# Kernel optimization log

Measured on AMD Instinct MI355X. Metric: run time of the kernel, lower is better.

The kernel has to match this reference:

```python
import jax, jax.numpy as jnp
import numpy as np

EPS = 1e-5

def _ln(x, g, b):
    # layer norm over last dim
    m = jnp.mean(x, axis=-1, keepdims=True)
    v = jnp.mean((x - m) ** 2, axis=-1, keepdims=True)
    return (x - m) * jax.lax.rsqrt(v + EPS) * g + b

def setup_inputs() -> dict:
    key = jax.random.key(0)
    ks = jax.random.split(key, 12)
    B, T, E, H, OUT = 128, 256, 64, 128, 1
    GENOME = 1_000_000
    D = 2 * E  # input_size_lstm
    inp = {}
    inp["indices"] = jax.random.randint(ks[0], (B, T, 2), 0, GENOME, dtype=jnp.int64)
    inp["h0"] = jax.random.normal(ks[1], (B, H), dtype=jnp.float32)
    inp["c0"] = jax.random.normal(ks[2], (B, H), dtype=jnp.float32)
    inp["embed_table"] = jax.random.normal(ks[3], (GENOME, E), dtype=jnp.float32)
    s_ih = 1.0 / np.sqrt(D)
    s_hh = 1.0 / np.sqrt(H)
    inp["W_ih"] = jax.random.uniform(ks[4], (4 * H, D), minval=-s_ih, maxval=s_ih, dtype=jnp.float32)
    inp["W_hh"] = jax.random.uniform(ks[5], (4 * H, H), minval=-s_hh, maxval=s_hh, dtype=jnp.float32)
    inp["g_ih"] = jnp.ones((4 * H,), jnp.float32)
    inp["b_ih"] = jnp.zeros((4 * H,), jnp.float32)
    inp["g_hh"] = jnp.ones((4 * H,), jnp.float32)
    inp["b_hh"] = jnp.zeros((4 * H,), jnp.float32)
    inp["g_c"] = jnp.ones((H,), jnp.float32)
    inp["b_c"] = jnp.zeros((H,), jnp.float32)
    s_o = 1.0 / np.sqrt(H * T)
    inp["W_out"] = jax.random.uniform(ks[6], (OUT * T, H * T), minval=-s_o, maxval=s_o, dtype=jnp.float32)
    inp["b_out"] = jax.random.uniform(ks[7], (OUT * T,), minval=-s_o, maxval=s_o, dtype=jnp.float32)
    return inp

def _forward(indices, embed_table, W_ih, W_hh, g_ih, b_ih, g_hh, b_hh, g_c, b_c, W_out, b_out, h0, c0):
    B, T = indices.shape[0], indices.shape[1]
    H = h0.shape[-1]
    # embedding gather: (B,T,2,E) -> (B,T,2E)
    emb = embed_table[indices].reshape(B, T, -1)
    # precompute input-to-hidden gates for all timesteps: (B,T,4H)
    x_gates = jnp.einsum("btd,gd->btg", emb, W_ih)

    def step(carry, xg):
        h, c = carry
        gates = _ln(xg, g_ih, b_ih) + _ln(h @ W_hh.T, g_hh, b_hh)
        i, f, g, o = jnp.split(gates, 4, axis=-1)
        c_new = jax.nn.sigmoid(f) * c + jax.nn.sigmoid(i) * jnp.tanh(g)
        h_new = jax.nn.sigmoid(o) * jnp.tanh(_ln(c_new, g_c, b_c))
        return (h_new, c_new), h_new

    (_, _), hs = jax.lax.scan(step, (h0, c0), jnp.swapaxes(x_gates, 0, 1))
    # hs: (T,B,H) -> (B,T*H)
    seq_out = jnp.swapaxes(hs, 0, 1).reshape(B, T * H)
    out = jax.nn.sigmoid(seq_out @ W_out.T + b_out)
    return out, emb

def reference(indices, h0, c0, embed_table, W_ih, W_hh, g_ih, b_ih, g_hh, b_hh, g_c, b_c, W_out, b_out):
    return _forward(indices, embed_table, W_ih, W_hh, g_ih, b_ih, g_hh, b_hh, g_c, b_c, W_out, b_out, h0, c0)
```

## Files before the change

kernel.cpp:

```cpp
#include <hip/hip_runtime.h>
#include <cstddef>


typedef __attribute__((ext_vector_type(8))) _Float16 f16x8;
typedef __attribute__((ext_vector_type(4))) float f32x4;

__device__ __forceinline__ float frcp(float x) { return __builtin_amdgcn_rcpf(x); }
__device__ __forceinline__ float sigm(float x) { return frcp(1.0f + __expf(-x)); }
__device__ __forceinline__ float ftanh(float x) {
  float e = __expf(2.0f * x);
  return (e - 1.0f) * frcp(e + 1.0f);
}
__device__ __forceinline__ void split2(float x, unsigned short& hi, unsigned short& lo) {
  _Float16 h = (_Float16)x;
  _Float16 l = (_Float16)((x - (float)h) * 2048.0f);
  hi = *(unsigned short*)&h;
  lo = *(unsigned short*)&l;
}
__device__ __forceinline__ void barrier_lds() {
  asm volatile("s_waitcnt lgkmcnt(0)\n\ts_barrier" ::: "memory");
}

#define SEL4(v, jj) ((jj) == 0 ? (v)[0] : (jj) == 1 ? (v)[1] : (jj) == 2 ? (v)[2] : (v)[3])

__global__ void k_embed(const int* __restrict__ idx, const float4* __restrict__ table4,
                        float4* __restrict__ emb4) {
  int i = blockIdx.x * blockDim.x + threadIdx.x;
  int p = i >> 4, j = i & 15;
  int id = idx[p];
  emb4[(size_t)p * 16 + j] = table4[(size_t)id * 16 + j];
}

__global__ __launch_bounds__(256) void k_gemm_tn(
    const float* __restrict__ A, const float* __restrict__ Bm, float* __restrict__ C,
    int K, int kchunks, int N, size_t partstride)
{
  __shared__ float As[64][65];
  __shared__ float Bs[64][68];
  const int tid = threadIdx.x;
  const int tx = tid & 15, ty = tid >> 4;
  const int m0 = blockIdx.x * 64, n0 = blockIdx.y * 64;
  float acc[4][4] = {};
  size_t kbase = (size_t)blockIdx.z * kchunks * 64;
  for (int kc = 0; kc < kchunks; ++kc) {
    size_t k0 = kbase + (size_t)kc * 64;
    #pragma unroll
    for (int it = 0; it < 4; ++it) {
      int fi = it * 256 + tid;
      int row = fi >> 4, col4 = fi & 15;
      float4 va = *(const float4*)(A + (size_t)(m0 + row) * K + k0 + col4 * 4);
      As[row][col4*4+0] = va.x; As[row][col4*4+1] = va.y;
      As[row][col4*4+2] = va.z; As[row][col4*4+3] = va.w;
      float4 vb = *(const float4*)(Bm + (size_t)(n0 + row) * K + k0 + col4 * 4);
      Bs[col4*4+0][row] = vb.x; Bs[col4*4+1][row] = vb.y;
      Bs[col4*4+2][row] = vb.z; Bs[col4*4+3][row] = vb.w;
    }
    __syncthreads();
    #pragma unroll 8
    for (int k = 0; k < 64; ++k) {
      float a0 = As[ty*4+0][k], a1 = As[ty*4+1][k], a2 = As[ty*4+2][k], a3 = As[ty*4+3][k];
      float b0 = Bs[k][tx*4+0], b1 = Bs[k][tx*4+1], b2 = Bs[k][tx*4+2], b3 = Bs[k][tx*4+3];
      acc[0][0] += a0*b0; acc[0][1] += a0*b1; acc[0][2] += a0*b2; acc[0][3] += a0*b3;
      acc[1][0] += a1*b0; acc[1][1] += a1*b1; acc[1][2] += a1*b2; acc[1][3] += a1*b3;
      acc[2][0] += a2*b0; acc[2][1] += a2*b1; acc[2][2] += a2*b2; acc[2][3] += a2*b3;
      acc[3][0] += a3*b0; acc[3][1] += a3*b1; acc[3][2] += a3*b2; acc[3][3] += a3*b3;
    }
    __syncthreads();
  }
  float* Cp = C + (size_t)blockIdx.z * partstride;
  #pragma unroll
  for (int i = 0; i < 4; ++i) {
    float4 v = make_float4(acc[i][0], acc[i][1], acc[i][2], acc[i][3]);
    *(float4*)(Cp + (size_t)(m0 + ty*4 + i) * N + n0 + tx*4) = v;
  }
}

__global__ __launch_bounds__(256) void k_xln(float4* __restrict__ xg4,
                                             const float4* __restrict__ g4,
                                             const float4* __restrict__ bi4,
                                             const float4* __restrict__ bh4) {
  int row = blockIdx.x * 4 + (threadIdx.x >> 6);
  int lane = threadIdx.x & 63;
  float4* r = xg4 + (size_t)row * 128;
  float4 a = r[lane], b = r[lane + 64];
  float s = a.x + a.y + a.z + a.w + b.x + b.y + b.z + b.w;
  float q = a.x*a.x + a.y*a.y + a.z*a.z + a.w*a.w + b.x*b.x + b.y*b.y + b.z*b.z + b.w*b.w;
  #pragma unroll
  for (int off = 32; off; off >>= 1) { s += __shfl_xor(s, off); q += __shfl_xor(q, off); }
  float m = s * (1.0f / 512.0f);
  float rs = rsqrtf(q * (1.0f / 512.0f) - m * m + 1e-5f);
  float4 ga = g4[lane], gb = g4[64 + lane];
  float4 ia = bi4[lane], ib = bi4[64 + lane];
  float4 ha = bh4[lane], hb = bh4[64 + lane];
  a.x = (a.x - m) * rs * ga.x + ia.x + ha.x; a.y = (a.y - m) * rs * ga.y + ia.y + ha.y;
  a.z = (a.z - m) * rs * ga.z + ia.z + ha.z; a.w = (a.w - m) * rs * ga.w + ia.w + ha.w;
  b.x = (b.x - m) * rs * gb.x + ib.x + hb.x; b.y = (b.y - m) * rs * gb.y + ib.y + hb.y;
  b.z = (b.z - m) * rs * gb.z + ib.z + hb.z; b.w = (b.w - m) * rs * gb.w + ib.w + hb.w;
  r[lane] = a; r[lane + 64] = b;
}

__global__ void k_wprep(const float* __restrict__ Whh, uint4* __restrict__ wfh,
                        uint4* __restrict__ wfl) {
  int i = blockIdx.x * 256 + threadIdx.x;
  int l = i & 63, kc = (i >> 6) & 3, mt = i >> 8;
  int row = mt * 16 + (l & 15);
  int kb = kc * 32 + 8 * (l >> 4);
  float4 a = *(const float4*)(Whh + row * 128 + kb);
  float4 c = *(const float4*)(Whh + row * 128 + kb + 4);
  unsigned short h0,h1,h2,h3,h4,h5,h6,h7, l0,l1,l2,l3,l4,l5,l6,l7;
  split2(a.x,h0,l0); split2(a.y,h1,l1); split2(a.z,h2,l2); split2(a.w,h3,l3);
  split2(c.x,h4,l4); split2(c.y,h5,l5); split2(c.z,h6,l6); split2(c.w,h7,l7);
  uint4 oh, ol;
  oh.x = h0 | ((unsigned)h1 << 16); oh.y = h2 | ((unsigned)h3 << 16);
  oh.z = h4 | ((unsigned)h5 << 16); oh.w = h6 | ((unsigned)h7 << 16);
  ol.x = l0 | ((unsigned)l1 << 16); ol.y = l2 | ((unsigned)l3 << 16);
  ol.z = l4 | ((unsigned)l5 << 16); ol.w = l6 | ((unsigned)l7 << 16);
  wfh[i] = oh; wfl[i] = ol;
}

__global__ __launch_bounds__(512, 2) void k_scan(
    const float* __restrict__ xln,
    const uint4* __restrict__ wfh,
    const uint4* __restrict__ wfl,
    const float* __restrict__ h0, const float* __restrict__ c0,
    const float* __restrict__ g_hh,
    const float* __restrict__ g_c,  const float* __restrict__ b_c,
    float* __restrict__ hs)
{
  const int b = blockIdx.x;
  const int tid = threadIdx.x;
  const int w = tid >> 6, l = tid & 63;
  const int lg = l >> 4;
  const int jj = (l & 15) >> 2;
  const bool wr = (l & 3) == 0;
  const int u = w * 16 + lg * 4 + jj;
  const float inv2048 = 1.0f / 2048.0f;

  __shared__ alignas(16) unsigned short hbh[128];
  __shared__ alignas(16) unsigned short hbl[128];
  __shared__ float2 hred[8];
  __shared__ float2 cred[8];

  uint4 afh0[4], afh1[4], afh2[4], afh3[4];
  uint4 afl0[4], afl1[4], afl2[4], afl3[4];
  #pragma unroll
  for (int kc = 0; kc < 4; ++kc) {
    afh0[kc] = wfh[((w     ) * 4 + kc) * 64 + l];
    afh1[kc] = wfh[((w +  8) * 4 + kc) * 64 + l];
    afh2[kc] = wfh[((w + 16) * 4 + kc) * 64 + l];
    afh3[kc] = wfh[((w + 24) * 4 + kc) * 64 + l];
    afl0[kc] = wfl[((w     ) * 4 + kc) * 64 + l];
    afl1[kc] = wfl[((w +  8) * 4 + kc) * 64 + l];
    afl2[kc] = wfl[((w + 16) * 4 + kc) * 64 + l];
    afl3[kc] = wfl[((w + 24) * 4 + kc) * 64 + l];
  }
  #pragma unroll
  for (int kc = 0; kc < 4; ++kc) {
    asm volatile("" : "+v"(afh0[kc].x), "+v"(afh0[kc].y), "+v"(afh0[kc].z), "+v"(afh0[kc].w));
    asm volatile("" : "+v"(afh1[kc].x), "+v"(afh1[kc].y), "+v"(afh1[kc].z), "+v"(afh1[kc].w));
    asm volatile("" : "+v"(afh2[kc].x), "+v"(afh2[kc].y), "+v"(afh2[kc].z), "+v"(afh2[kc].w));
    asm volatile("" : "+v"(afh3[kc].x), "+v"(afh3[kc].y), "+v"(afh3[kc].z), "+v"(afh3[kc].w));
    asm volatile("" : "+v"(afl0[kc].x), "+v"(afl0[kc].y), "+v"(afl0[kc].z), "+v"(afl0[kc].w));
    asm volatile("" : "+v"(afl1[kc].x), "+v"(afl1[kc].y), "+v"(afl1[kc].z), "+v"(afl1[kc].w));
    asm volatile("" : "+v"(afl2[kc].x), "+v"(afl2[kc].y), "+v"(afl2[kc].z), "+v"(afl2[kc].w));
    asm volatile("" : "+v"(afl3[kc].x), "+v"(afl3[kc].y), "+v"(afl3[kc].z), "+v"(afl3[kc].w));
  }

  const float ghI = g_hh[u], ghF = g_hh[128 + u], ghG = g_hh[256 + u], ghO = g_hh[384 + u];
  const float gcv = g_c[u], bcv = b_c[u];
  float cv = c0[b * 128 + u];
  if (wr) {
    unsigned short hi, lo;
    split2(h0[b * 128 + u], hi, lo);
    hbh[u] = hi; hbl[u] = lo;
  }
  __syncthreads();

  const float* xgb = xln + (size_t)b * 256 * 512;
  float* hsb = hs + (size_t)b * 256 * 128;

  float xI = xgb[u], xF = xgb[128 + u], xG = xgb[256 + u], xO = xgb[384 + u];

  for (int t = 0; t < 256; ++t) {
    const float* xn = xgb + (((t + 1) & 255) << 9);
    float nI = xn[u], nF = xn[128 + u], nG = xn[256 + u], nO = xn[384 + u];

    f32x4 acc0 = {0,0,0,0}, acc1 = {0,0,0,0}, acc2 = {0,0,0,0}, acc3 = {0,0,0,0};
    f32x4 e0 = {0,0,0,0}, e1 = {0,0,0,0}, e2 = {0,0,0,0}, e3 = {0,0,0,0};
    #pragma unroll
    for (int kc = 0; kc < 4; ++kc) {
      uint4 buh = *(const uint4*)((const char*)hbh + kc * 64 + 16 * lg);
      uint4 bul = *(const uint4*)((const char*)hbl + kc * 64 + 16 * lg);
      f16x8 bh = *(f16x8*)&buh;
      f16x8 bl = *(f16x8*)&bul;
      acc0 = __builtin_amdgcn_mfma_f32_16x16x32_f16(*(f16x8*)&afh0[kc], bh, acc0, 0, 0, 0);
      acc1 = __builtin_amdgcn_mfma_f32_16x16x32_f16(*(f16x8*)&afh1[kc], bh, acc1, 0, 0, 0);
      acc2 = __builtin_amdgcn_mfma_f32_16x16x32_f16(*(f16x8*)&afh2[kc], bh, acc2, 0, 0, 0);
      acc3 = __builtin_amdgcn_mfma_f32_16x16x32_f16(*(f16x8*)&afh3[kc], bh, acc3, 0, 0, 0);
      e0 = __builtin_amdgcn_mfma_f32_16x16x32_f16(*(f16x8*)&afh0[kc], bl, e0, 0, 0, 0);
      e1 = __builtin_amdgcn_mfma_f32_16x16x32_f16(*(f16x8*)&afh1[kc], bl, e1, 0, 0, 0);
      e2 = __builtin_amdgcn_mfma_f32_16x16x32_f16(*(f16x8*)&afh2[kc], bl, e2, 0, 0, 0);
      e3 = __builtin_amdgcn_mfma_f32_16x16x32_f16(*(f16x8*)&afh3[kc], bl, e3, 0, 0, 0);
      e0 = __builtin_amdgcn_mfma_f32_16x16x32_f16(*(f16x8*)&afl0[kc], bh, e0, 0, 0, 0);
      e1 = __builtin_amdgcn_mfma_f32_16x16x32_f16(*(f16x8*)&afl1[kc], bh, e1, 0, 0, 0);
      e2 = __builtin_amdgcn_mfma_f32_16x16x32_f16(*(f16x8*)&afl2[kc], bh, e2, 0, 0, 0);
      e3 = __builtin_amdgcn_mfma_f32_16x16x32_f16(*(f16x8*)&afl3[kc], bh, e3, 0, 0, 0);
    }
    f32x4 a0, a1, a2, a3;
    #pragma unroll
    for (int j = 0; j < 4; ++j) {
      a0[j] = acc0[j] + e0[j] * inv2048;
      a1[j] = acc1[j] + e1[j] * inv2048;
      a2[j] = acc2[j] + e2[j] * inv2048;
      a3[j] = acc3[j] + e3[j] * inv2048;
    }

    float s = 0.f, q = 0.f;
    #pragma unroll
    for (int j = 0; j < 4; ++j) {
      s += a0[j] + a1[j] + a2[j] + a3[j];
      q += a0[j]*a0[j] + a1[j]*a1[j] + a2[j]*a2[j] + a3[j]*a3[j];
    }
    s += __shfl_xor(s, 16); s += __shfl_xor(s, 32);
    q += __shfl_xor(q, 16); q += __shfl_xor(q, 32);
    if (l == 0) hred[w] = make_float2(s, q);

    barrier_lds();

    float rsx = 0.f, rsq = 0.f;
    #pragma unroll
    for (int i = 0; i < 8; ++i) { float2 v = hred[i]; rsx += v.x; rsq += v.y; }
    float mh = rsx * (1.0f / 512.0f);
    float rh = rsqrtf(rsq * (1.0f / 512.0f) - mh * mh + 1e-5f);

    float aI = SEL4(a0, jj), aF = SEL4(a1, jj), aG = SEL4(a2, jj), aO = SEL4(a3, jj);
    float gI = xI + (aI - mh) * rh * ghI;
    float gF = xF + (aF - mh) * rh * ghF;
    float gG = xG + (aG - mh) * rh * ghG;
    float gO = xO + (aO - mh) * rh * ghO;

    float cn = sigm(gF) * cv + sigm(gI) * ftanh(gG);
    cv = cn;

    float cs = cn, cq = cn * cn;
    #pragma unroll
    for (int off = 32; off; off >>= 1) { cs += __shfl_xor(cs, off); cq += __shfl_xor(cq, off); }
    if (l == 0) cred[w] = make_float2(cs, cq);

    barrier_lds();

    float tcs = 0.f, tcq = 0.f;
    #pragma unroll
    for (int i = 0; i < 8; ++i) { float2 v = cred[i]; tcs += v.x; tcq += v.y; }
    float mc = tcs * (1.0f / 512.0f);
    float rc = rsqrtf(tcq * (1.0f / 512.0f) - mc * mc + 1e-5f);

    float lnc = (cn - mc) * rc * gcv + bcv;
    float hn = sigm(gO) * ftanh(lnc);

    if (wr) {
      unsigned short hi, lo;
      split2(hn, hi, lo);
      hbh[u] = hi; hbl[u] = lo;
      hsb[(size_t)t * 128 + u] = hn;
    }
    xI = nI; xF = nF; xG = nG; xO = nO;

    barrier_lds();
  }
}

__global__ void k_reduce(const float* __restrict__ part, const float* __restrict__ b_out,
                         float* __restrict__ out) {
  int i = blockIdx.x * 256 + threadIdx.x;
  float s = b_out[i & 255];
  #pragma unroll
  for (int z = 0; z < 32; ++z) s += part[(size_t)z * 32768 + i];
  out[i] = sigm(s);
}

extern "C" void kernel_launch(void* const* d_in, const int* in_sizes, int n_in,
                              void* d_out, int out_size, void* d_ws, size_t ws_size,
                              hipStream_t stream) {
  const int*   idx   = (const int*)  d_in[0];
  const float* h0    = (const float*)d_in[1];
  const float* c0    = (const float*)d_in[2];
  const float* table = (const float*)d_in[3];
  const float* W_ih  = (const float*)d_in[4];
  const float* W_hh  = (const float*)d_in[5];
  const float* g_ih  = (const float*)d_in[6];
  const float* b_ih  = (const float*)d_in[7];
  const float* g_hh  = (const float*)d_in[8];
  const float* b_hh  = (const float*)d_in[9];
  const float* g_c   = (const float*)d_in[10];
  const float* b_c   = (const float*)d_in[11];
  const float* W_out = (const float*)d_in[12];
  const float* b_out = (const float*)d_in[13];

  float* out  = (float*)d_out;
  float* emb  = out + 32768;
  float* ws   = (float*)d_ws;
  float* xg   = ws;
  float* hsb  = ws + 16777216;
  uint4* wfh  = (uint4*)(ws + 20971520);
  uint4* wfl  = (uint4*)(ws + 21004288);
  float* part = ws + 21037056;

  k_embed<<<4096, 256, 0, stream>>>(idx, (const float4*)table, (float4*)emb);
  k_gemm_tn<<<dim3(512, 8, 1), 256, 0, stream>>>(emb, W_ih, xg, 128, 2, 512, 0);
  k_xln<<<8192, 256, 0, stream>>>((float4*)xg, (const float4*)g_ih,
                                  (const float4*)b_ih, (const float4*)b_hh);
  k_wprep<<<32, 256, 0, stream>>>(W_hh, wfh, wfl);
  k_scan<<<128, 512, 0, stream>>>(xg, wfh, wfl, h0, c0, g_hh, g_c, b_c, hsb);
  k_gemm_tn<<<dim3(2, 4, 32), 256, 0, stream>>>(hsb, W_out, part, 32768, 16, 256, 32768);
  k_reduce<<<128, 256, 0, stream>>>(part, b_out, out);
}
```

Measured before the change: 649.4 us.

## Batch four sequences per scan block using spare MFMA columns

The recurrent scan kernel now handles four batch rows per workgroup instead of one. The h-state B operand is laid out so that four of the sixteen MFMA N columns carry distinct batch rows, where before all columns held the same vector. Each lane now processes four hidden units with vectorised loads and stores, and the launch drops from 128 to 32 blocks. The recurrent weight fragments are also pinned to accumulator registers. This cuts redundant matrix and memory work per sequence, at the cost of more elementwise work per lane on the serial per-step critical path and fewer active CUs.

```diff
diff --git a/kernel.cpp b/kernel.cpp
--- a/kernel.cpp
+++ b/kernel.cpp
@@ -20,8 +20,6 @@
 __device__ __forceinline__ void barrier_lds() {
   asm volatile("s_waitcnt lgkmcnt(0)\n\ts_barrier" ::: "memory");
 }
-
-#define SEL4(v, jj) ((jj) == 0 ? (v)[0] : (jj) == 1 ? (v)[1] : (jj) == 2 ? (v)[2] : (v)[3])
 
 __global__ void k_embed(const int* __restrict__ idx, const float4* __restrict__ table4,
                         float4* __restrict__ emb4) {
@@ -127,84 +125,97 @@
     const float* __restrict__ g_c,  const float* __restrict__ b_c,
     float* __restrict__ hs)
 {
-  const int b = blockIdx.x;
+  const int bid = blockIdx.x;
   const int tid = threadIdx.x;
   const int w = tid >> 6, l = tid & 63;
   const int lg = l >> 4;
-  const int jj = (l & 15) >> 2;
-  const bool wr = (l & 3) == 0;
-  const int u = w * 16 + lg * 4 + jj;
+  const int col = l & 15;
+  const bool act = col < 4;
+  const int rclamp = act ? col : 0;
+  const int row = bid * 4 + rclamp;
+  const int u0 = 16 * w + 4 * lg;
   const float inv2048 = 1.0f / 2048.0f;
 
-  __shared__ alignas(16) unsigned short hbh[128];
-  __shared__ alignas(16) unsigned short hbl[128];
-  __shared__ float2 hred[8];
-  __shared__ float2 cred[8];
-
-  uint4 afh0[4], afh1[4], afh2[4], afh3[4];
-  uint4 afl0[4], afl1[4], afl2[4], afl3[4];
+  __shared__ alignas(16) unsigned short hsth[2048];
+  __shared__ alignas(16) unsigned short hstl[2048];
+  __shared__ float2 hred[8][16];
+  __shared__ float2 cred[8][16];
+
+  const f16x8* wh8 = (const f16x8*)wfh;
+  const f16x8* wl8 = (const f16x8*)wfl;
+  f16x8 AH0[4], AH1[4], AH2[4], AH3[4], AL0[4], AL1[4], AL2[4], AL3[4];
   #pragma unroll
   for (int kc = 0; kc < 4; ++kc) {
-    afh0[kc] = wfh[((w     ) * 4 + kc) * 64 + l];
-    afh1[kc] = wfh[((w +  8) * 4 + kc) * 64 + l];
-    afh2[kc] = wfh[((w + 16) * 4 + kc) * 64 + l];
-    afh3[kc] = wfh[((w + 24) * 4 + kc) * 64 + l];
-    afl0[kc] = wfl[((w     ) * 4 + kc) * 64 + l];
-    afl1[kc] = wfl[((w +  8) * 4 + kc) * 64 + l];
-    afl2[kc] = wfl[((w + 16) * 4 + kc) * 64 + l];
-    afl3[kc] = wfl[((w + 24) * 4 + kc) * 64 + l];
+    AH0[kc] = wh8[((w     ) * 4 + kc) * 64 + l];
+    AH1[kc] = wh8[((w +  8) * 4 + kc) * 64 + l];
+    AH2[kc] = wh8[((w + 16) * 4 + kc) * 64 + l];
+    AH3[kc] = wh8[((w + 24) * 4 + kc) * 64 + l];
+    AL0[kc] = wl8[((w     ) * 4 + kc) * 64 + l];
+    AL1[kc] = wl8[((w +  8) * 4 + kc) * 64 + l];
+    AL2[kc] = wl8[((w + 16) * 4 + kc) * 64 + l];
+    AL3[kc] = wl8[((w + 24) * 4 + kc) * 64 + l];
   }
   #pragma unroll
   for (int kc = 0; kc < 4; ++kc) {
-    asm volatile("" : "+v"(afh0[kc].x), "+v"(afh0[kc].y), "+v"(afh0[kc].z), "+v"(afh0[kc].w));
-    asm volatile("" : "+v"(afh1[kc].x), "+v"(afh1[kc].y), "+v"(afh1[kc].z), "+v"(afh1[kc].w));
-    asm volatile("" : "+v"(afh2[kc].x), "+v"(afh2[kc].y), "+v"(afh2[kc].z), "+v"(afh2[kc].w));
-    asm volatile("" : "+v"(afh3[kc].x), "+v"(afh3[kc].y), "+v"(afh3[kc].z), "+v"(afh3[kc].w));
-    asm volatile("" : "+v"(afl0[kc].x), "+v"(afl0[kc].y), "+v"(afl0[kc].z), "+v"(afl0[kc].w));
-    asm volatile("" : "+v"(afl1[kc].x), "+v"(afl1[kc].y), "+v"(afl1[kc].z), "+v"(afl1[kc].w));
-    asm volatile("" : "+v"(afl2[kc].x), "+v"(afl2[kc].y), "+v"(afl2[kc].z), "+v"(afl2[kc].w));
-    asm volatile("" : "+v"(afl3[kc].x), "+v"(afl3[kc].y), "+v"(afl3[kc].z), "+v"(afl3[kc].w));
-  }
-
-  const float ghI = g_hh[u], ghF = g_hh[128 + u], ghG = g_hh[256 + u], ghO = g_hh[384 + u];
-  const float gcv = g_c[u], bcv = b_c[u];
-  float cv = c0[b * 128 + u];
-  if (wr) {
-    unsigned short hi, lo;
-    split2(h0[b * 128 + u], hi, lo);
-    hbh[u] = hi; hbl[u] = lo;
-  }
+    asm volatile("" : "+a"(AH0[kc]), "+a"(AH1[kc]), "+a"(AH2[kc]), "+a"(AH3[kc]));
+    asm volatile("" : "+a"(AL0[kc]), "+a"(AL1[kc]), "+a"(AL2[kc]), "+a"(AL3[kc]));
+  }
+
+  const f32x4 ghI = *(const f32x4*)(g_hh + u0);
+  const f32x4 ghF = *(const f32x4*)(g_hh + 128 + u0);
+  const f32x4 ghG = *(const f32x4*)(g_hh + 256 + u0);
+  const f32x4 ghO = *(const f32x4*)(g_hh + 384 + u0);
+  const f32x4 gc4 = *(const f32x4*)(g_c + u0);
+  const f32x4 bc4 = *(const f32x4*)(b_c + u0);
+  f32x4 cv = *(const f32x4*)(c0 + (size_t)row * 128 + u0);
+
+  #pragma unroll
+  for (int i = tid; i < 1024; i += 512) {
+    ((unsigned int*)hsth)[i] = 0u;
+    ((unsigned int*)hstl)[i] = 0u;
+  }
+  const int kcb = u0 >> 5, lg2 = (u0 >> 3) & 3, i0 = u0 & 7;
+  const int wroff = kcb * 1024 + (lg2 * 16 + col) * 16 + i0 * 2;
   __syncthreads();
-
-  const float* xgb = xln + (size_t)b * 256 * 512;
-  float* hsb = hs + (size_t)b * 256 * 128;
-
-  float xI = xgb[u], xF = xgb[128 + u], xG = xgb[256 + u], xO = xgb[384 + u];
+  if (act) {
+    f32x4 h04 = *(const f32x4*)(h0 + (size_t)row * 128 + u0);
+    unsigned short a_, b_, c_, d_, e_, f_, g_, i_;
+    split2(h04[0], a_, b_); split2(h04[1], c_, d_);
+    split2(h04[2], e_, f_); split2(h04[3], g_, i_);
+    uint2 hv; hv.x = (unsigned)a_ | ((unsigned)c_ << 16); hv.y = (unsigned)e_ | ((unsigned)g_ << 16);
+    uint2 lv; lv.x = (unsigned)b_ | ((unsigned)d_ << 16); lv.y = (unsigned)f_ | ((unsigned)i_ << 16);
+    *(uint2*)((char*)hsth + wroff) = hv;
+    *(uint2*)((char*)hstl + wroff) = lv;
+  }
+  __syncthreads();
+
+  const float* xgb = xln + (size_t)row * 131072;
+  float* hsb = hs + (size_t)row * 32768;
+
+  f32x4 xI = *(const f32x4*)(xgb + u0);
+  f32x4 xF = *(const f32x4*)(xgb + 128 + u0);
+  f32x4 xG = *(const f32x4*)(xgb + 256 + u0);
+  f32x4 xO = *(const f32x4*)(xgb + 384 + u0);
 
   for (int t = 0; t < 256; ++t) {
-    const float* xn = xgb + (((t + 1) & 255) << 9);
-    float nI = xn[u], nF = xn[128 + u], nG = xn[256 + u], nO = xn[384 + u];
-
     f32x4 acc0 = {0,0,0,0}, acc1 = {0,0,0,0}, acc2 = {0,0,0,0}, acc3 = {0,0,0,0};
     f32x4 e0 = {0,0,0,0}, e1 = {0,0,0,0}, e2 = {0,0,0,0}, e3 = {0,0,0,0};
     #pragma unroll
     for (int kc = 0; kc < 4; ++kc) {
-      uint4 buh = *(const uint4*)((const char*)hbh + kc * 64 + 16 * lg);
-      uint4 bul = *(const uint4*)((const char*)hbl + kc * 64 + 16 * lg);
-      f16x8 bh = *(f16x8*)&buh;
-      f16x8 bl = *(f16x8*)&bul;
-      acc0 = __builtin_amdgcn_mfma_f32_16x16x32_f16(*(f16x8*)&afh0[kc], bh, acc0, 0, 0, 0);
-      acc1 = __builtin_amdgcn_mfma_f32_16x16x32_f16(*(f16x8*)&afh1[kc], bh, acc1, 0, 0, 0);
-      acc2 = __builtin_amdgcn_mfma_f32_16x16x32_f16(*(f16x8*)&afh2[kc], bh, acc2, 0, 0, 0);
-      acc3 = __builtin_amdgcn_mfma_f32_16x16x32_f16(*(f16x8*)&afh3[kc], bh, acc3, 0, 0, 0);
-      e0 = __builtin_amdgcn_mfma_f32_16x16x32_f16(*(f16x8*)&afh0[kc], bl, e0, 0, 0, 0);
-      e1 = __builtin_amdgcn_mfma_f32_16x16x32_f16(*(f16x8*)&afh1[kc], bl, e1, 0, 0, 0);
-      e2 = __builtin_amdgcn_mfma_f32_16x16x32_f16(*(f16x8*)&afh2[kc], bl, e2, 0, 0, 0);
-      e3 = __builtin_amdgcn_mfma_f32_16x16x32_f16(*(f16x8*)&afh3[kc], bl, e3, 0, 0, 0);
-      e0 = __builtin_amdgcn_mfma_f32_16x16x32_f16(*(f16x8*)&afl0[kc], bh, e0, 0, 0, 0);
-      e1 = __builtin_amdgcn_mfma_f32_16x16x32_f16(*(f16x8*)&afl1[kc], bh, e1, 0, 0, 0);
-      e2 = __builtin_amdgcn_mfma_f32_16x16x32_f16(*(f16x8*)&afl2[kc], bh, e2, 0, 0, 0);
-      e3 = __builtin_amdgcn_mfma_f32_16x16x32_f16(*(f16x8*)&afl3[kc], bh, e3, 0, 0, 0);
+      f16x8 bh = *(const f16x8*)((const char*)hsth + kc * 1024 + l * 16);
+      f16x8 bl = *(const f16x8*)((const char*)hstl + kc * 1024 + l * 16);
+      acc0 = __builtin_amdgcn_mfma_f32_16x16x32_f16(AH0[kc], bh, acc0, 0, 0, 0);
+      acc1 = __builtin_amdgcn_mfma_f32_16x16x32_f16(AH1[kc], bh, acc1, 0, 0, 0);
+      acc2 = __builtin_amdgcn_mfma_f32_16x16x32_f16(AH2[kc], bh, acc2, 0, 0, 0);
+      acc3 = __builtin_amdgcn_mfma_f32_16x16x32_f16(AH3[kc], bh, acc3, 0, 0, 0);
+      e0 = __builtin_amdgcn_mfma_f32_16x16x32_f16(AH0[kc], bl, e0, 0, 0, 0);
+      e1 = __builtin_amdgcn_mfma_f32_16x16x32_f16(AH1[kc], bl, e1, 0, 0, 0);
+      e2 = __builtin_amdgcn_mfma_f32_16x16x32_f16(AH2[kc], bl, e2, 0, 0, 0);
+      e3 = __builtin_amdgcn_mfma_f32_16x16x32_f16(AH3[kc], bl, e3, 0, 0, 0);
+      e0 = __builtin_amdgcn_mfma_f32_16x16x32_f16(AL0[kc], bh, e0, 0, 0, 0);
+      e1 = __builtin_amdgcn_mfma_f32_16x16x32_f16(AL1[kc], bh, e1, 0, 0, 0);
+      e2 = __builtin_amdgcn_mfma_f32_16x16x32_f16(AL2[kc], bh, e2, 0, 0, 0);
+      e3 = __builtin_amdgcn_mfma_f32_16x16x32_f16(AL3[kc], bh, e3, 0, 0, 0);
     }
     f32x4 a0, a1, a2, a3;
     #pragma unroll
@@ -223,48 +234,61 @@
     }
     s += __shfl_xor(s, 16); s += __shfl_xor(s, 32);
     q += __shfl_xor(q, 16); q += __shfl_xor(q, 32);
-    if (l == 0) hred[w] = make_float2(s, q);
+    if (l < 4) hred[w][l] = make_float2(s, q);
 
     barrier_lds();
 
     float rsx = 0.f, rsq = 0.f;
     #pragma unroll
-    for (int i = 0; i < 8; ++i) { float2 v = hred[i]; rsx += v.x; rsq += v.y; }
+    for (int w2 = 0; w2 < 8; ++w2) { float2 v = hred[w2][col]; rsx += v.x; rsq += v.y; }
     float mh = rsx * (1.0f / 512.0f);
     float rh = rsqrtf(rsq * (1.0f / 512.0f) - mh * mh + 1e-5f);
 
-    float aI = SEL4(a0, jj), aF = SEL4(a1, jj), aG = SEL4(a2, jj), aO = SEL4(a3, jj);
-    float gI = xI + (aI - mh) * rh * ghI;
-    float gF = xF + (aF - mh) * rh * ghF;
-    float gG = xG + (aG - mh) * rh * ghG;
-    float gO = xO + (aO - mh) * rh * ghO;
-
-    float cn = sigm(gF) * cv + sigm(gI) * ftanh(gG);
-    cv = cn;
-
-    float cs = cn, cq = cn * cn;
-    #pragma unroll
-    for (int off = 32; off; off >>= 1) { cs += __shfl_xor(cs, off); cq += __shfl_xor(cq, off); }
-    if (l == 0) cred[w] = make_float2(cs, cq);
+    f32x4 cn;
+    float cs = 0.f, cq = 0.f;
+    #pragma unroll
+    for (int j = 0; j < 4; ++j) {
+      float gI = xI[j] + (a0[j] - mh) * rh * ghI[j];
+      float gF = xF[j] + (a1[j] - mh) * rh * ghF[j];
+      float gG = xG[j] + (a2[j] - mh) * rh * ghG[j];
+      float gO = xO[j] + (a3[j] - mh) * rh * ghO[j];
+      float c_ = sigm(gF) * cv[j] + sigm(gI) * ftanh(gG);
+      cn[j] = c_; cv[j] = c_;
+      xO[j] = gO;
+      cs += c_; cq += c_ * c_;
+    }
+    cs += __shfl_xor(cs, 16); cs += __shfl_xor(cs, 32);
+    cq += __shfl_xor(cq, 16); cq += __shfl_xor(cq, 32);
+    if (l < 4) cred[w][l] = make_float2(cs, cq);
 
     barrier_lds();
 
     float tcs = 0.f, tcq = 0.f;
     #pragma unroll
-    for (int i = 0; i < 8; ++i) { float2 v = cred[i]; tcs += v.x; tcq += v.y; }
-    float mc = tcs * (1.0f / 512.0f);
-    float rc = rsqrtf(tcq * (1.0f / 512.0f) - mc * mc + 1e-5f);
-
-    float lnc = (cn - mc) * rc * gcv + bcv;
-    float hn = sigm(gO) * ftanh(lnc);
-
-    if (wr) {
-      unsigned short hi, lo;
-      split2(hn, hi, lo);
-      hbh[u] = hi; hbl[u] = lo;
-      hsb[(size_t)t * 128 + u] = hn;
-    }
-    xI = nI; xF = nF; xG = nG; xO = nO;
+    for (int w2 = 0; w2 < 8; ++w2) { float2 v = cred[w2][col]; tcs += v.x; tcq += v.y; }
+    float mc = tcs * (1.0f / 128.0f);
+    float rc = rsqrtf(tcq * (1.0f / 128.0f) - mc * mc + 1e-5f);
+
+    f32x4 hn;
+    #pragma unroll
+    for (int j = 0; j < 4; ++j)
+      hn[j] = sigm(xO[j]) * ftanh((cn[j] - mc) * rc * gc4[j] + bc4[j]);
+
+    if (act) {
+      unsigned short a_, b_, c_, d_, e_, f_, g_, i_;
+      split2(hn[0], a_, b_); split2(hn[1], c_, d_);
+      split2(hn[2], e_, f_); split2(hn[3], g_, i_);
+      uint2 hv; hv.x = (unsigned)a_ | ((unsigned)c_ << 16); hv.y = (unsigned)e_ | ((unsigned)g_ << 16);
+      uint2 lv; lv.x = (unsigned)b_ | ((unsigned)d_ << 16); lv.y = (unsigned)f_ | ((unsigned)i_ << 16);
+      *(uint2*)((char*)hsth + wroff) = hv;
+      *(uint2*)((char*)hstl + wroff) = lv;
+      *(f32x4*)(hsb + (size_t)t * 128 + u0) = hn;
+    }
+    const float* xn = xgb + (size_t)((t + 1) & 255) * 512;
+    xI = *(const f32x4*)(xn + u0);
+    xF = *(const f32x4*)(xn + 128 + u0);
+    xG = *(const f32x4*)(xn + 256 + u0);
+    xO = *(const f32x4*)(xn + 384 + u0);
 
     barrier_lds();
   }
@@ -311,7 +335,7 @@
   k_xln<<<8192, 256, 0, stream>>>((float4*)xg, (const float4*)g_ih,
                                   (const float4*)b_ih, (const float4*)b_hh);
   k_wprep<<<32, 256, 0, stream>>>(W_hh, wfh, wfl);
-  k_scan<<<128, 512, 0, stream>>>(xg, wfh, wfl, h0, c0, g_hh, g_c, b_c, hsb);
+  k_scan<<<32, 512, 0, stream>>>(xg, wfh, wfl, h0, c0, g_hh, g_c, b_c, hsb);
   k_gemm_tn<<<dim3(2, 4, 32), 256, 0, stream>>>(hsb, W_out, part, 32768, 16, 256, 32768);
   k_reduce<<<128, 256, 0, stream>>>(part, b_out, out);
 }
```

New measurement: 1.010 ms. +55.5%, slower.

## Halve scan block to 4 waves and drop per-step third barrier

Applied to the files above, without the earlier changes.

The recurrent scan kernel now uses 256 threads (4 waves) per batch row instead of 512, with each wave holding twice as many W_hh fragments in registers and issuing twice as many MFMAs per step. Each wave keeps its own private copy of h in LDS, so the end-of-step barrier is removed and each step needs two barriers instead of three. The cell-state layer norm is now computed by every wave redundantly, reading the staged c and o values from a shared buffer. The costs are higher register pressure from 128 fragment registers per lane, and fewer waves on each CU to hide MFMA and transcendental latency.

```diff
diff --git a/kernel.cpp b/kernel.cpp
--- a/kernel.cpp
+++ b/kernel.cpp
@@ -22,6 +22,7 @@
 }
 
 #define SEL4(v, jj) ((jj) == 0 ? (v)[0] : (jj) == 1 ? (v)[1] : (jj) == 2 ? (v)[2] : (v)[3])
+#define MFMA16(a, b, c) __builtin_amdgcn_mfma_f32_16x16x32_f16((a), (b), (c), 0, 0, 0)
 
 __global__ void k_embed(const int* __restrict__ idx, const float4* __restrict__ table4,
                         float4* __restrict__ emb4) {
@@ -118,10 +119,10 @@
   wfh[i] = oh; wfl[i] = ol;
 }
 
-__global__ __launch_bounds__(512, 2) void k_scan(
+__global__ __launch_bounds__(256, 1) void k_scan(
     const float* __restrict__ xln,
-    const uint4* __restrict__ wfh,
-    const uint4* __restrict__ wfl,
+    const f16x8* __restrict__ wfh,
+    const f16x8* __restrict__ wfl,
     const float* __restrict__ h0, const float* __restrict__ c0,
     const float* __restrict__ g_hh,
     const float* __restrict__ g_c,  const float* __restrict__ b_c,
@@ -131,142 +132,143 @@
   const int tid = threadIdx.x;
   const int w = tid >> 6, l = tid & 63;
   const int lg = l >> 4;
-  const int jj = (l & 15) >> 2;
-  const bool wr = (l & 3) == 0;
-  const int u = w * 16 + lg * 4 + jj;
+  const int col = l & 15;
+  const int msel = (col >> 2) & 1;
+  const int j = col & 3;
+  const bool own = col < 8;
+  const int u = ((w + 4 * msel) << 4) + 4 * lg + j;
   const float inv2048 = 1.0f / 2048.0f;
 
-  __shared__ alignas(16) unsigned short hbh[128];
-  __shared__ alignas(16) unsigned short hbl[128];
-  __shared__ float2 hred[8];
-  __shared__ float2 cred[8];
-
-  uint4 afh0[4], afh1[4], afh2[4], afh3[4];
-  uint4 afl0[4], afl1[4], afl2[4], afl3[4];
+  __shared__ alignas(16) unsigned short hwh[4][128];
+  __shared__ alignas(16) unsigned short hwl[4][128];
+  __shared__ alignas(16) float2 cbuf[128];
+  __shared__ alignas(16) float2 hred[4];
+  __shared__ alignas(16) float2 cstat[4];
+
+  f16x8 HI0[4], HI1[4], HF0[4], HF1[4], HG0[4], HG1[4], HO0[4], HO1[4];
+  f16x8 LI0[4], LI1[4], LF0[4], LF1[4], LG0[4], LG1[4], LO0[4], LO1[4];
   #pragma unroll
   for (int kc = 0; kc < 4; ++kc) {
-    afh0[kc] = wfh[((w     ) * 4 + kc) * 64 + l];
-    afh1[kc] = wfh[((w +  8) * 4 + kc) * 64 + l];
-    afh2[kc] = wfh[((w + 16) * 4 + kc) * 64 + l];
-    afh3[kc] = wfh[((w + 24) * 4 + kc) * 64 + l];
-    afl0[kc] = wfl[((w     ) * 4 + kc) * 64 + l];
-    afl1[kc] = wfl[((w +  8) * 4 + kc) * 64 + l];
-    afl2[kc] = wfl[((w + 16) * 4 + kc) * 64 + l];
-    afl3[kc] = wfl[((w + 24) * 4 + kc) * 64 + l];
-  }
-  #pragma unroll
-  for (int kc = 0; kc < 4; ++kc) {
-    asm volatile("" : "+v"(afh0[kc].x), "+v"(afh0[kc].y), "+v"(afh0[kc].z), "+v"(afh0[kc].w));
-    asm volatile("" : "+v"(afh1[kc].x), "+v"(afh1[kc].y), "+v"(afh1[kc].z), "+v"(afh1[kc].w));
-    asm volatile("" : "+v"(afh2[kc].x), "+v"(afh2[kc].y), "+v"(afh2[kc].z), "+v"(afh2[kc].w));
-    asm volatile("" : "+v"(afh3[kc].x), "+v"(afh3[kc].y), "+v"(afh3[kc].z), "+v"(afh3[kc].w));
-    asm volatile("" : "+v"(afl0[kc].x), "+v"(afl0[kc].y), "+v"(afl0[kc].z), "+v"(afl0[kc].w));
-    asm volatile("" : "+v"(afl1[kc].x), "+v"(afl1[kc].y), "+v"(afl1[kc].z), "+v"(afl1[kc].w));
-    asm volatile("" : "+v"(afl2[kc].x), "+v"(afl2[kc].y), "+v"(afl2[kc].z), "+v"(afl2[kc].w));
-    asm volatile("" : "+v"(afl3[kc].x), "+v"(afl3[kc].y), "+v"(afl3[kc].z), "+v"(afl3[kc].w));
+    HI0[kc] = wfh[((w     ) * 4 + kc) * 64 + l];
+    HI1[kc] = wfh[((w +  4) * 4 + kc) * 64 + l];
+    HF0[kc] = wfh[((w +  8) * 4 + kc) * 64 + l];
+    HF1[kc] = wfh[((w + 12) * 4 + kc) * 64 + l];
+    HG0[kc] = wfh[((w + 16) * 4 + kc) * 64 + l];
+    HG1[kc] = wfh[((w + 20) * 4 + kc) * 64 + l];
+    HO0[kc] = wfh[((w + 24) * 4 + kc) * 64 + l];
+    HO1[kc] = wfh[((w + 28) * 4 + kc) * 64 + l];
+    LI0[kc] = wfl[((w     ) * 4 + kc) * 64 + l];
+    LI1[kc] = wfl[((w +  4) * 4 + kc) * 64 + l];
+    LF0[kc] = wfl[((w +  8) * 4 + kc) * 64 + l];
+    LF1[kc] = wfl[((w + 12) * 4 + kc) * 64 + l];
+    LG0[kc] = wfl[((w + 16) * 4 + kc) * 64 + l];
+    LG1[kc] = wfl[((w + 20) * 4 + kc) * 64 + l];
+    LO0[kc] = wfl[((w + 24) * 4 + kc) * 64 + l];
+    LO1[kc] = wfl[((w + 28) * 4 + kc) * 64 + l];
   }
 
   const float ghI = g_hh[u], ghF = g_hh[128 + u], ghG = g_hh[256 + u], ghO = g_hh[384 + u];
-  const float gcv = g_c[u], bcv = b_c[u];
   float cv = c0[b * 128 + u];
-  if (wr) {
-    unsigned short hi, lo;
-    split2(h0[b * 128 + u], hi, lo);
-    hbh[u] = hi; hbl[u] = lo;
-  }
-  __syncthreads();
-
-  const float* xgb = xln + (size_t)b * 256 * 512;
-  float* hsb = hs + (size_t)b * 256 * 128;
+  const float gcA = g_c[2*l], gcB = g_c[2*l+1], bcA = b_c[2*l], bcB = b_c[2*l+1];
+
+  {
+    float2 h2 = *(const float2*)(h0 + b * 128 + 2 * l);
+    unsigned short a_, b_, c_, d_;
+    split2(h2.x, a_, b_); split2(h2.y, c_, d_);
+    *(unsigned int*)&hwh[w][2*l] = (unsigned)a_ | ((unsigned)c_ << 16);
+    *(unsigned int*)&hwl[w][2*l] = (unsigned)b_ | ((unsigned)d_ << 16);
+  }
+
+  const float* xgb = xln + (size_t)b * 131072;
+  float* hsb = hs + (size_t)b * 32768;
 
   float xI = xgb[u], xF = xgb[128 + u], xG = xgb[256 + u], xO = xgb[384 + u];
 
   for (int t = 0; t < 256; ++t) {
-    const float* xn = xgb + (((t + 1) & 255) << 9);
-    float nI = xn[u], nF = xn[128 + u], nG = xn[256 + u], nO = xn[384 + u];
-
-    f32x4 acc0 = {0,0,0,0}, acc1 = {0,0,0,0}, acc2 = {0,0,0,0}, acc3 = {0,0,0,0};
-    f32x4 e0 = {0,0,0,0}, e1 = {0,0,0,0}, e2 = {0,0,0,0}, e3 = {0,0,0,0};
+    asm volatile("s_waitcnt lgkmcnt(0)" ::: "memory");
+    f32x4 aI0 = {0,0,0,0}, aI1 = {0,0,0,0}, aF0 = {0,0,0,0}, aF1 = {0,0,0,0};
+    f32x4 aG0 = {0,0,0,0}, aG1 = {0,0,0,0}, aO0 = {0,0,0,0}, aO1 = {0,0,0,0};
+    f32x4 eI0 = {0,0,0,0}, eI1 = {0,0,0,0}, eF0 = {0,0,0,0}, eF1 = {0,0,0,0};
+    f32x4 eG0 = {0,0,0,0}, eG1 = {0,0,0,0}, eO0 = {0,0,0,0}, eO1 = {0,0,0,0};
     #pragma unroll
     for (int kc = 0; kc < 4; ++kc) {
-      uint4 buh = *(const uint4*)((const char*)hbh + kc * 64 + 16 * lg);
-      uint4 bul = *(const uint4*)((const char*)hbl + kc * 64 + 16 * lg);
-      f16x8 bh = *(f16x8*)&buh;
-      f16x8 bl = *(f16x8*)&bul;
-      acc0 = __builtin_amdgcn_mfma_f32_16x16x32_f16(*(f16x8*)&afh0[kc], bh, acc0, 0, 0, 0);
-      acc1 = __builtin_amdgcn_mfma_f32_16x16x32_f16(*(f16x8*)&afh1[kc], bh, acc1, 0, 0, 0);
-      acc2 = __builtin_amdgcn_mfma_f32_16x16x32_f16(*(f16x8*)&afh2[kc], bh, acc2, 0, 0, 0);
-      acc3 = __builtin_amdgcn_mfma_f32_16x16x32_f16(*(f16x8*)&afh3[kc], bh, acc3, 0, 0, 0);
-      e0 = __builtin_amdgcn_mfma_f32_16x16x32_f16(*(f16x8*)&afh0[kc], bl, e0, 0, 0, 0);
-      e1 = __builtin_amdgcn_mfma_f32_16x16x32_f16(*(f16x8*)&afh1[kc], bl, e1, 0, 0, 0);
-      e2 = __builtin_amdgcn_mfma_f32_16x16x32_f16(*(f16x8*)&afh2[kc], bl, e2, 0, 0, 0);
-      e3 = __builtin_amdgcn_mfma_f32_16x16x32_f16(*(f16x8*)&afh3[kc], bl, e3, 0, 0, 0);
-      e0 = __builtin_amdgcn_mfma_f32_16x16x32_f16(*(f16x8*)&afl0[kc], bh, e0, 0, 0, 0);
-      e1 = __builtin_amdgcn_mfma_f32_16x16x32_f16(*(f16x8*)&afl1[kc], bh, e1, 0, 0, 0);
-      e2 = __builtin_amdgcn_mfma_f32_16x16x32_f16(*(f16x8*)&afl2[kc], bh, e2, 0, 0, 0);
-      e3 = __builtin_amdgcn_mfma_f32_16x16x32_f16(*(f16x8*)&afl3[kc], bh, e3, 0, 0, 0);
+      f16x8 bh = *(const f16x8*)((const char*)&hwh[w][0] + kc * 64 + 16 * lg);
+      f16x8 bl = *(const f16x8*)((const char*)&hwl[w][0] + kc * 64 + 16 * lg);
+      aI0 = MFMA16(HI0[kc], bh, aI0); eI0 = MFMA16(HI0[kc], bl, eI0); eI0 = MFMA16(LI0[kc], bh, eI0);
+      aI1 = MFMA16(HI1[kc], bh, aI1); eI1 = MFMA16(HI1[kc], bl, eI1); eI1 = MFMA16(LI1[kc], bh, eI1);
+      aF0 = MFMA16(HF0[kc], bh, aF0); eF0 = MFMA16(HF0[kc], bl, eF0); eF0 = MFMA16(LF0[kc], bh, eF0);
+      aF1 = MFMA16(HF1[kc], bh, aF1); eF1 = MFMA16(HF1[kc], bl, eF1); eF1 = MFMA16(LF1[kc], bh, eF1);
+      aG0 = MFMA16(HG0[kc], bh, aG0); eG0 = MFMA16(HG0[kc], bl, eG0); eG0 = MFMA16(LG0[kc], bh, eG0);
+      aG1 = MFMA16(HG1[kc], bh, aG1); eG1 = MFMA16(HG1[kc], bl, eG1); eG1 = MFMA16(LG1[kc], bh, eG1);
+      aO0 = MFMA16(HO0[kc], bh, aO0); eO0 = MFMA16(HO0[kc], bl, eO0); eO0 = MFMA16(LO0[kc], bh, eO0);
+      aO1 = MFMA16(HO1[kc], bh, aO1); eO1 = MFMA16(HO1[kc], bl, eO1); eO1 = MFMA16(LO1[kc], bh, eO1);
     }
-    f32x4 a0, a1, a2, a3;
-    #pragma unroll
-    for (int j = 0; j < 4; ++j) {
-      a0[j] = acc0[j] + e0[j] * inv2048;
-      a1[j] = acc1[j] + e1[j] * inv2048;
-      a2[j] = acc2[j] + e2[j] * inv2048;
-      a3[j] = acc3[j] + e3[j] * inv2048;
-    }
-
-    float s = 0.f, q = 0.f;
-    #pragma unroll
-    for (int j = 0; j < 4; ++j) {
-      s += a0[j] + a1[j] + a2[j] + a3[j];
-      q += a0[j]*a0[j] + a1[j]*a1[j] + a2[j]*a2[j] + a3[j]*a3[j];
-    }
+    aI0 += eI0 * inv2048; aI1 += eI1 * inv2048;
+    aF0 += eF0 * inv2048; aF1 += eF1 * inv2048;
+    aG0 += eG0 * inv2048; aG1 += eG1 * inv2048;
+    aO0 += eO0 * inv2048; aO1 += eO1 * inv2048;
+
+    f32x4 sv = ((aI0 + aI1) + (aF0 + aF1)) + ((aG0 + aG1) + (aO0 + aO1));
+    f32x4 qv = ((aI0*aI0 + aI1*aI1) + (aF0*aF0 + aF1*aF1)) +
+               ((aG0*aG0 + aG1*aG1) + (aO0*aO0 + aO1*aO1));
+    float s = (sv[0] + sv[1]) + (sv[2] + sv[3]);
+    float q = (qv[0] + qv[1]) + (qv[2] + qv[3]);
     s += __shfl_xor(s, 16); s += __shfl_xor(s, 32);
     q += __shfl_xor(q, 16); q += __shfl_xor(q, 32);
     if (l == 0) hred[w] = make_float2(s, q);
 
     barrier_lds();
 
-    float rsx = 0.f, rsq = 0.f;
-    #pragma unroll
-    for (int i = 0; i < 8; ++i) { float2 v = hred[i]; rsx += v.x; rsq += v.y; }
-    float mh = rsx * (1.0f / 512.0f);
-    float rh = rsqrtf(rsq * (1.0f / 512.0f) - mh * mh + 1e-5f);
-
-    float aI = SEL4(a0, jj), aF = SEL4(a1, jj), aG = SEL4(a2, jj), aO = SEL4(a3, jj);
-    float gI = xI + (aI - mh) * rh * ghI;
-    float gF = xF + (aF - mh) * rh * ghF;
-    float gG = xG + (aG - mh) * rh * ghG;
-    float gO = xO + (aO - mh) * rh * ghO;
+    float4 hp0 = *(const float4*)&hred[0];
+    float4 hp1 = *(const float4*)&hred[2];
+    float mh = ((hp0.x + hp0.z) + (hp1.x + hp1.z)) * (1.0f / 512.0f);
+    float vq = ((hp0.y + hp0.w) + (hp1.y + hp1.w)) * (1.0f / 512.0f) - mh * mh;
+    float rh = rsqrtf(vq + 1e-5f);
+
+    float aIv = msel ? SEL4(aI1, j) : SEL4(aI0, j);
+    float aFv = msel ? SEL4(aF1, j) : SEL4(aF0, j);
+    float aGv = msel ? SEL4(aG1, j) : SEL4(aG0, j);
+    float aOv = msel ? SEL4(aO1, j) : SEL4(aO0, j);
+
+    float gI = xI + (aIv - mh) * rh * ghI;
+    float gF = xF + (aFv - mh) * rh * ghF;
+    float gG = xG + (aGv - mh) * rh * ghG;
+    float gO = xO + (aOv - mh) * rh * ghO;
 
     float cn = sigm(gF) * cv + sigm(gI) * ftanh(gG);
     cv = cn;
 
-    float cs = cn, cq = cn * cn;
-    #pragma unroll
-    for (int off = 32; off; off >>= 1) { cs += __shfl_xor(cs, off); cq += __shfl_xor(cq, off); }
-    if (l == 0) cred[w] = make_float2(cs, cq);
+    float cs = own ? cn : 0.f, cq = own ? cn * cn : 0.f;
+    cs += __shfl_xor(cs, 1); cq += __shfl_xor(cq, 1);
+    cs += __shfl_xor(cs, 2); cq += __shfl_xor(cq, 2);
+    cs += __shfl_xor(cs, 4); cq += __shfl_xor(cq, 4);
+    cs += __shfl_xor(cs, 16); cq += __shfl_xor(cq, 16);
+    cs += __shfl_xor(cs, 32); cq += __shfl_xor(cq, 32);
+    if (l == 0) cstat[w] = make_float2(cs, cq);
+    if (own) cbuf[u] = make_float2(cn, gO);
 
     barrier_lds();
 
-    float tcs = 0.f, tcq = 0.f;
-    #pragma unroll
-    for (int i = 0; i < 8; ++i) { float2 v = cred[i]; tcs += v.x; tcq += v.y; }
-    float mc = tcs * (1.0f / 512.0f);
-    float rc = rsqrtf(tcq * (1.0f / 512.0f) - mc * mc + 1e-5f);
-
-    float lnc = (cn - mc) * rc * gcv + bcv;
-    float hn = sigm(gO) * ftanh(lnc);
-
-    if (wr) {
-      unsigned short hi, lo;
-      split2(hn, hi, lo);
-      hbh[u] = hi; hbl[u] = lo;
-      hsb[(size_t)t * 128 + u] = hn;
+    float4 cp0 = *(const float4*)&cstat[0];
+    float4 cp1 = *(const float4*)&cstat[2];
+    float mc = ((cp0.x + cp0.z) + (cp1.x + cp1.z)) * (1.0f / 128.0f);
+    float vc = ((cp0.y + cp0.w) + (cp1.y + cp1.w)) * (1.0f / 128.0f) - mc * mc;
+    float rc = rsqrtf(vc + 1e-5f);
+
+    float4 cb = *(const float4*)&cbuf[2 * l];
+    float hn0 = sigm(cb.y) * ftanh((cb.x - mc) * rc * gcA + bcA);
+    float hn1 = sigm(cb.w) * ftanh((cb.z - mc) * rc * gcB + bcB);
+
+    {
+      unsigned short a_, b_, c_, d_;
+      split2(hn0, a_, b_); split2(hn1, c_, d_);
+      *(unsigned int*)&hwh[w][2*l] = (unsigned)a_ | ((unsigned)c_ << 16);
+      *(unsigned int*)&hwl[w][2*l] = (unsigned)b_ | ((unsigned)d_ << 16);
     }
-    xI = nI; xF = nF; xG = nG; xO = nO;
-
-    barrier_lds();
+    if (w == 0) *(float2*)(hsb + (size_t)t * 128 + 2 * l) = make_float2(hn0, hn1);
+
+    const float* xn = xgb + (size_t)((t + 1) & 255) * 512;
+    xI = xn[u]; xF = xn[128 + u]; xG = xn[256 + u]; xO = xn[384 + u];
   }
 }
 
@@ -311,7 +313,8 @@
   k_xln<<<8192, 256, 0, stream>>>((float4*)xg, (const float4*)g_ih,
                                   (const float4*)b_ih, (const float4*)b_hh);
   k_wprep<<<32, 256, 0, stream>>>(W_hh, wfh, wfl);
-  k_scan<<<128, 512, 0, stream>>>(xg, wfh, wfl, h0, c0, g_hh, g_c, b_c, hsb);
+  k_scan<<<128, 256, 0, stream>>>(xg, (const f16x8*)wfh, (const f16x8*)wfl,
+                                  h0, c0, g_hh, g_c, b_c, hsb);
   k_gemm_tn<<<dim3(2, 4, 32), 256, 0, stream>>>(hsb, W_out, part, 32768, 16, 256, 32768);
   k_reduce<<<128, 256, 0, stream>>>(part, b_out, out);
 }
```

New measurement: 715.1 us. 1.1x slower.
